# Optimization experiments

Hardware: AMD Instinct MI355X
Metric: run time of the kernel (lower is better)

## Reference

```python
import jax, jax.numpy as jnp
import numpy as np

D = 768
HEAD_SIZE = 64  # D / num_heads = 768 / 12

def setup_inputs() -> dict:
    key = jax.random.key(0)
    k1, k2, k3, k4 = jax.random.split(key, 4)
    ix = jax.random.normal(k1, (8, 4096, D), dtype=jnp.float32)
    # Linear(D, head_size, bias=False) weights; stored as [D, head_size] for x @ W
    scale = 1.0 / np.sqrt(D)
    Wk = jax.random.uniform(k2, (D, HEAD_SIZE), dtype=jnp.float32, minval=-scale, maxval=scale)
    Wq = jax.random.uniform(k3, (D, HEAD_SIZE), dtype=jnp.float32, minval=-scale, maxval=scale)
    Wv = jax.random.uniform(k4, (D, HEAD_SIZE), dtype=jnp.float32, minval=-scale, maxval=scale)
    return {"ix": ix, "Wk": Wk, "Wq": Wq, "Wv": Wv}

def reference(ix, Wk, Wq, Wv):
    # ix: [B, S, D]
    k = ix @ Wk  # [B, S, H]
    q = ix @ Wq  # [B, S, H]
    v = ix @ Wv  # [B, S, H]
    scale = 1.0 / jnp.sqrt(jnp.asarray(HEAD_SIZE, ix.dtype))
    wei = jnp.einsum('bsh,bth->bst', q, k) * scale  # [B, S, S]
    wei = jax.nn.softmax(wei, axis=-1)
    out = jnp.einsum('bst,bth->bsh', wei, v)  # [B, S, H]
    return out
```

## Files before the change

kernel.cpp:

```cpp
#include <hip/hip_runtime.h>
#include <hip/hip_bf16.h>

#define D_DIM 768
#define HS 64
#define SEQ 4096
#define NBATCH 8

typedef short bf8 __attribute__((ext_vector_type(8)));
typedef short bf4 __attribute__((ext_vector_type(4)));
typedef float f4 __attribute__((ext_vector_type(4)));

static __device__ __forceinline__ short f2b(float x) {
    __hip_bfloat16 h = __float2bfloat16(x);
    return __builtin_bit_cast(short, h);
}
static __device__ __forceinline__ unsigned pk2(float x, float y) {
    unsigned ux = __builtin_bit_cast(unsigned, x) + 0x8000u;
    unsigned uy = __builtin_bit_cast(unsigned, y) + 0x8000u;
    return __builtin_amdgcn_perm(uy, ux, 0x07060302u);
}

#if defined(__has_builtin)
#if __has_builtin(__builtin_amdgcn_exp2f)
#define EXP2F(x) __builtin_amdgcn_exp2f(x)
#endif
#endif
#ifndef EXP2F
#define EXP2F(x) exp2f(x)
#endif

__global__ __launch_bounds__(256) void wconv_kernel(
    const float* __restrict__ Wk, const float* __restrict__ Wq,
    const float* __restrict__ Wv, short* __restrict__ wt)
{
    int tid = blockIdx.x * 256 + threadIdx.x;
    int mat = tid / (D_DIM * HS);
    int rem = tid - mat * (D_DIM * HS);
    int k = rem >> 6;
    int n = rem & 63;
    const float* W = (mat == 0) ? Wk : (mat == 1) ? Wq : Wv;
    float scale = (mat == 1) ? 0.18033688011112042f : 1.0f;
    wt[(mat * HS + n) * D_DIM + k] = f2b(W[rem] * scale);
}

__global__ __launch_bounds__(256) void proj_kernel(
    const float* __restrict__ ix, const short* __restrict__ wt,
    short* __restrict__ qg, short* __restrict__ kg, short* __restrict__ vg)
{
    __shared__ short ixl[2][32 * 40];
    __shared__ short wtl[2][192 * 40];

    const int t = threadIdx.x;
    const int wave = t >> 6, lane = t & 63;
    const int m = lane & 15, quad = lane >> 4;
    const int m0 = blockIdx.x * 32;

    const int srow = t >> 3;
    const int skoff = (t & 7) * 4;

    f4 xr;
    bf8 wr0, wr1, wr2, wr3;

    auto load_chunk = [&](int c) {
        const float* px = ix + (m0 + srow) * D_DIM + c * 32 + skoff;
        xr = *(const f4*)px;
        if (t < 192) {
            const short* pw = wt + t * D_DIM + c * 32;
            wr0 = *(const bf8*)(pw);
            wr1 = *(const bf8*)(pw + 8);
            wr2 = *(const bf8*)(pw + 16);
            wr3 = *(const bf8*)(pw + 24);
        }
    };
    auto write_chunk = [&](int p) {
        bf4 xw;
        #pragma unroll
        for (int i = 0; i < 4; ++i) xw[i] = f2b(xr[i]);
        *(bf4*)(&ixl[p][srow * 40 + skoff]) = xw;
        if (t < 192) {
            *(bf8*)(&wtl[p][t * 40 + 0])  = wr0;
            *(bf8*)(&wtl[p][t * 40 + 8])  = wr1;
            *(bf8*)(&wtl[p][t * 40 + 16]) = wr2;
            *(bf8*)(&wtl[p][t * 40 + 24]) = wr3;
        }
    };

    f4 acc[2][3] = {};

    load_chunk(0); write_chunk(0); __syncthreads();

    for (int c = 0; c < 24; ++c) {
        const int p = c & 1;
        if (c + 1 < 24) load_chunk(c + 1);

        bf8 a0 = *(const bf8*)(&ixl[p][(m) * 40 + quad * 8]);
        bf8 a1 = *(const bf8*)(&ixl[p][(16 + m) * 40 + quad * 8]);
        bf8 bb[3];
        #pragma unroll
        for (int nt = 0; nt < 3; ++nt)
            bb[nt] = *(const bf8*)(&wtl[p][(wave * 48 + nt * 16 + m) * 40 + quad * 8]);
        #pragma unroll
        for (int nt = 0; nt < 3; ++nt) {
            acc[0][nt] = __builtin_amdgcn_mfma_f32_16x16x32_bf16(a0, bb[nt], acc[0][nt], 0, 0, 0);
            acc[1][nt] = __builtin_amdgcn_mfma_f32_16x16x32_bf16(a1, bb[nt], acc[1][nt], 0, 0, 0);
        }

        if (c + 1 < 24) { write_chunk((c + 1) & 1); __syncthreads(); }
    }

    #pragma unroll
    for (int mt = 0; mt < 2; ++mt) {
        const int row = m0 + mt * 16 + quad * 4;
        #pragma unroll
        for (int nt = 0; nt < 3; ++nt) {
            const int cb = wave * 48 + nt * 16;
            short* op = (cb < 64) ? kg : (cb < 128) ? qg : vg;
            const int n = (cb & 63) + m;
            #pragma unroll
            for (int r = 0; r < 4; ++r)
                op[(row + r) * HS + n] = f2b(acc[mt][nt][r]);
        }
    }
}

__global__ __launch_bounds__(256, 4) void attn_kernel(
    const short* __restrict__ qg, const short* __restrict__ kg,
    const short* __restrict__ vg, float* __restrict__ num0,
    float* __restrict__ num1, float* __restrict__ num2,
    float* __restrict__ num3, float* __restrict__ den0,
    float* __restrict__ den1, float* __restrict__ den2,
    float* __restrict__ den3)
{
    __shared__ short kl[2][64 * 72];
    __shared__ short vl[2][64 * 64];

    const int t = threadIdx.x;
    const int wave = t >> 6, lane = t & 63;
    const int m = lane & 15, quad = lane >> 4;

    const int flat = blockIdx.x;
    const int lg = (flat & 7) * 128 + (flat >> 3);
    const int qx = lg & 31;
    const int ks = (lg >> 5) & 3;
    const int b  = lg >> 7;

    const int rbase = b * SEQ;
    const int kbase = rbase + ks * (SEQ / 4);
    const int qw = qx * 128 + wave * 32;

    float* __restrict__ nump = (ks == 0) ? num0 : (ks == 1) ? num1 : (ks == 2) ? num2 : num3;
    float* __restrict__ denp = (ks == 0) ? den0 : (ks == 1) ? den1 : (ks == 2) ? den2 : den3;

    bf8 qf[2][2];
    #pragma unroll
    for (int nq = 0; nq < 2; ++nq)
        #pragma unroll
        for (int st = 0; st < 2; ++st)
            qf[nq][st] = *(const bf8*)(qg + (rbase + qw + nq * 16 + m) * HS + st * 32 + quad * 8);

    const int srow = t >> 2, soff = (t & 3) * 16;
    const int jp = t >> 3, dg = t & 7;
    const int j0 = jp * 2;
    const int jj = j0 & 31;
    const int gj = j0 >> 5;
    const int vq = (jj >> 2) & 3;
    const int vh = (jj >> 4) & 1;
    const int vb = (jj & 3) >> 1;
    const int vcol_base = vh * 4 + 2 * vb;
    const int vchunk_l = 4 * gj + vq;

    uint4 kr0, kr1, vr0, vr1;
    auto load_chunk = [&](int c) {
        const short* pk = kg + (kbase + c * 64 + srow) * HS + soff;
        kr0 = *(const uint4*)pk; kr1 = *(const uint4*)(pk + 8);
        const short* pv = vg + (kbase + c * 64 + j0) * HS + dg * 8;
        vr0 = *(const uint4*)pv; vr1 = *(const uint4*)(pv + HS);
    };
    auto write_chunk = [&](int p) {
        *(bf8*)(&kl[p][srow * 72 + soff])     = __builtin_bit_cast(bf8, kr0);
        *(bf8*)(&kl[p][srow * 72 + soff + 8]) = __builtin_bit_cast(bf8, kr1);
        bf8 v0 = __builtin_bit_cast(bf8, vr0), v1 = __builtin_bit_cast(bf8, vr1);
        #pragma unroll
        for (int i = 0; i < 8; ++i) {
            const int d = dg * 8 + i;
            const int chunk = vchunk_l ^ (i ^ dg);
            unsigned val = (unsigned short)v0[i] | ((unsigned)(unsigned short)v1[i] << 16);
            *(unsigned*)(&vl[p][d * 64 + chunk * 8 + vcol_base]) = val;
        }
    };

    f4 o[2][4] = {};
    float den[2] = {0.f, 0.f};

    load_chunk(0); write_chunk(0); __syncthreads();

    const int NCH = SEQ / 4 / 64;
    for (int c = 0; c < NCH; ++c) {
        const int p = c & 1;
        if (c + 1 < NCH) load_chunk(c + 1);

        #pragma unroll
        for (int g = 0; g < 2; ++g) {
            bf8 kA0 = *(const bf8*)(&kl[p][(g * 32 + m) * 72 + quad * 8]);
            bf8 kA1 = *(const bf8*)(&kl[p][(g * 32 + m) * 72 + 32 + quad * 8]);
            bf8 kB0 = *(const bf8*)(&kl[p][(g * 32 + 16 + m) * 72 + quad * 8]);
            bf8 kB1 = *(const bf8*)(&kl[p][(g * 32 + 16 + m) * 72 + 32 + quad * 8]);

            bf8 vf[4];
            #pragma unroll
            for (int dt = 0; dt < 4; ++dt) {
                const int row = dt * 16 + m;
                const int key = (m & 7) ^ (2 * dt + (m >> 3));
                const int chunk = (g * 4 + quad) ^ key;
                vf[dt] = *(const bf8*)(&vl[p][row * 64 + chunk * 8]);
            }

            #pragma unroll
            for (int nq = 0; nq < 2; ++nq) {
                f4 sa = {0.f, 0.f, 0.f, 0.f}, sb = {0.f, 0.f, 0.f, 0.f};
                sa = __builtin_amdgcn_mfma_f32_16x16x32_bf16(kA0, qf[nq][0], sa, 0, 0, 0);
                sa = __builtin_amdgcn_mfma_f32_16x16x32_bf16(kA1, qf[nq][1], sa, 0, 0, 0);
                sb = __builtin_amdgcn_mfma_f32_16x16x32_bf16(kB0, qf[nq][0], sb, 0, 0, 0);
                sb = __builtin_amdgcn_mfma_f32_16x16x32_bf16(kB1, qf[nq][1], sb, 0, 0, 0);
                float e0 = EXP2F(sa[0]), e1 = EXP2F(sa[1]), e2 = EXP2F(sa[2]), e3 = EXP2F(sa[3]);
                float e4 = EXP2F(sb[0]), e5 = EXP2F(sb[1]), e6 = EXP2F(sb[2]), e7 = EXP2F(sb[3]);
                den[nq] += ((e0 + e1) + (e2 + e3)) + ((e4 + e5) + (e6 + e7));
                uint4 pu;
                pu.x = pk2(e0, e1); pu.y = pk2(e2, e3);
                pu.z = pk2(e4, e5); pu.w = pk2(e6, e7);
                bf8 pf = __builtin_bit_cast(bf8, pu);
                #pragma unroll
                for (int dt = 0; dt < 4; ++dt)
                    o[nq][dt] = __builtin_amdgcn_mfma_f32_16x16x32_bf16(vf[dt], pf, o[nq][dt], 0, 0, 0);
            }
        }

        if (c + 1 < NCH) { write_chunk((c + 1) & 1); __syncthreads(); }
    }

    #pragma unroll
    for (int nq = 0; nq < 2; ++nq) {
        float d = den[nq];
        d += __shfl_xor(d, 16, 64);
        d += __shfl_xor(d, 32, 64);
        const int orow = rbase + qw + nq * 16 + m;
        if (quad == 0) denp[orow] = d;
        #pragma unroll
        for (int dt = 0; dt < 4; ++dt)
            *(f4*)(nump + orow * HS + dt * 16 + quad * 4) = o[nq][dt];
    }
}

__global__ __launch_bounds__(256) void reduce_kernel(
    float* __restrict__ out, const float* __restrict__ num1,
    const float* __restrict__ num2, const float* __restrict__ num3,
    const float* __restrict__ den0, const float* __restrict__ den1,
    const float* __restrict__ den2, const float* __restrict__ den3)
{
    const int gid = blockIdx.x * 256 + threadIdx.x;
    const int base = gid * 4;
    const int r = base >> 6;
    f4 n0 = *(const f4*)(out + base);
    f4 n1 = *(const f4*)(num1 + base);
    f4 n2 = *(const f4*)(num2 + base);
    f4 n3 = *(const f4*)(num3 + base);
    const float rs = 1.0f / ((den0[r] + den1[r]) + (den2[r] + den3[r]));
    f4 res;
    #pragma unroll
    for (int i = 0; i < 4; ++i) res[i] = ((n0[i] + n1[i]) + (n2[i] + n3[i])) * rs;
    *(f4*)(out + base) = res;
}

extern "C" void kernel_launch(void* const* d_in, const int* in_sizes, int n_in,
                              void* d_out, int out_size, void* d_ws, size_t ws_size,
                              hipStream_t stream) {
    const float* ix = (const float*)d_in[0];
    const float* Wk = (const float*)d_in[1];
    const float* Wq = (const float*)d_in[2];
    const float* Wv = (const float*)d_in[3];
    float* out = (float*)d_out;

    const size_t NQKV = (size_t)NBATCH * SEQ * HS;
    short* qg = (short*)d_ws;
    short* kg = qg + NQKV;
    short* vg = kg + NQKV;
    short* wt = vg + NQKV;
    char*  fbase = (char*)(wt + 3 * D_DIM * HS);
    float* num1 = (float*)fbase;
    float* num2 = num1 + NQKV;
    float* num3 = num2 + NQKV;
    float* den0 = num3 + NQKV;
    float* den1 = den0 + (size_t)NBATCH * SEQ;
    float* den2 = den1 + (size_t)NBATCH * SEQ;
    float* den3 = den2 + (size_t)NBATCH * SEQ;

    wconv_kernel<<<(3 * D_DIM * HS) / 256, 256, 0, stream>>>(Wk, Wq, Wv, wt);
    proj_kernel<<<(NBATCH * SEQ) / 32, 256, 0, stream>>>(ix, wt, qg, kg, vg);
    attn_kernel<<<1024, 256, 0, stream>>>(qg, kg, vg, out, num1, num2, num3,
                                          den0, den1, den2, den3);
    reduce_kernel<<<(int)(NQKV / (256 * 4)), 256, 0, stream>>>(
        out, num1, num2, num3, den0, den1, den2, den3);
}
```

Before: 249.4 us.

## Pre-tile projection weights for direct MFMA loads and double the K chunk

Result: faster. 219.7 us (-11.9%).

```diff
diff --git a/kernel.cpp b/kernel.cpp
--- a/kernel.cpp
+++ b/kernel.cpp
@@ -31,7 +31,7 @@
 
 __global__ __launch_bounds__(256) void wconv_kernel(
     const float* __restrict__ Wk, const float* __restrict__ Wq,
-    const float* __restrict__ Wv, short* __restrict__ wt)
+    const float* __restrict__ Wv, short* __restrict__ wt3)
 {
     int tid = blockIdx.x * 256 + threadIdx.x;
     int mat = tid / (D_DIM * HS);
@@ -40,15 +40,16 @@
     int n = rem & 63;
     const float* W = (mat == 0) ? Wk : (mat == 1) ? Wq : Wv;
     float scale = (mat == 1) ? 0.18033688011112042f : 1.0f;
-    wt[(mat * HS + n) * D_DIM + k] = f2b(W[rem] * scale);
+    int cc = mat * HS + n;
+    int c = k >> 5, q = (k >> 3) & 3, e = k & 7;
+    wt3[(c * 192 + cc) * 32 + q * 8 + e] = f2b(W[rem] * scale);
 }
 
 __global__ __launch_bounds__(256) void proj_kernel(
-    const float* __restrict__ ix, const short* __restrict__ wt,
+    const float* __restrict__ ix, const short* __restrict__ wt3,
     short* __restrict__ qg, short* __restrict__ kg, short* __restrict__ vg)
 {
-    __shared__ short ixl[2][32 * 40];
-    __shared__ short wtl[2][192 * 40];
+    __shared__ short ixl[2][32 * 72];
 
     const int t = threadIdx.x;
     const int wave = t >> 6, lane = t & 63;
@@ -56,56 +57,51 @@
     const int m0 = blockIdx.x * 32;
 
     const int srow = t >> 3;
-    const int skoff = (t & 7) * 4;
-
-    f4 xr;
-    bf8 wr0, wr1, wr2, wr3;
-
-    auto load_chunk = [&](int c) {
-        const float* px = ix + (m0 + srow) * D_DIM + c * 32 + skoff;
-        xr = *(const f4*)px;
-        if (t < 192) {
-            const short* pw = wt + t * D_DIM + c * 32;
-            wr0 = *(const bf8*)(pw);
-            wr1 = *(const bf8*)(pw + 8);
-            wr2 = *(const bf8*)(pw + 16);
-            wr3 = *(const bf8*)(pw + 24);
-        }
-    };
-    auto write_chunk = [&](int p) {
-        bf4 xw;
-        #pragma unroll
-        for (int i = 0; i < 4; ++i) xw[i] = f2b(xr[i]);
-        *(bf4*)(&ixl[p][srow * 40 + skoff]) = xw;
-        if (t < 192) {
-            *(bf8*)(&wtl[p][t * 40 + 0])  = wr0;
-            *(bf8*)(&wtl[p][t * 40 + 8])  = wr1;
-            *(bf8*)(&wtl[p][t * 40 + 16]) = wr2;
-            *(bf8*)(&wtl[p][t * 40 + 24]) = wr3;
-        }
-    };
-
+    const int skoff = (t & 7) * 8;
+
+    f4 xr0, xr1;
+    auto load_ix = [&](int c) {
+        const float* px = ix + (m0 + srow) * D_DIM + c * 64 + skoff;
+        xr0 = *(const f4*)px;
+        xr1 = *(const f4*)(px + 4);
+    };
+    auto write_ix = [&](int p) {
+        bf8 xw;
+        #pragma unroll
+        for (int i = 0; i < 4; ++i) { xw[i] = f2b(xr0[i]); xw[i + 4] = f2b(xr1[i]); }
+        *(bf8*)(&ixl[p][srow * 72 + skoff]) = xw;
+    };
+
+    const int colb = wave * 48;
     f4 acc[2][3] = {};
 
-    load_chunk(0); write_chunk(0); __syncthreads();
-
-    for (int c = 0; c < 24; ++c) {
+    load_ix(0); write_ix(0); __syncthreads();
+
+    for (int c = 0; c < 12; ++c) {
         const int p = c & 1;
-        if (c + 1 < 24) load_chunk(c + 1);
-
-        bf8 a0 = *(const bf8*)(&ixl[p][(m) * 40 + quad * 8]);
-        bf8 a1 = *(const bf8*)(&ixl[p][(16 + m) * 40 + quad * 8]);
-        bf8 bb[3];
-        #pragma unroll
-        for (int nt = 0; nt < 3; ++nt)
-            bb[nt] = *(const bf8*)(&wtl[p][(wave * 48 + nt * 16 + m) * 40 + quad * 8]);
+        if (c + 1 < 12) load_ix(c + 1);
+
+        bf8 b0[3], b1[3];
         #pragma unroll
         for (int nt = 0; nt < 3; ++nt) {
-            acc[0][nt] = __builtin_amdgcn_mfma_f32_16x16x32_bf16(a0, bb[nt], acc[0][nt], 0, 0, 0);
-            acc[1][nt] = __builtin_amdgcn_mfma_f32_16x16x32_bf16(a1, bb[nt], acc[1][nt], 0, 0, 0);
-        }
-
-        if (c + 1 < 24) { write_chunk((c + 1) & 1); __syncthreads(); }
+            const short* pw = wt3 + ((2 * c) * 192 + colb + nt * 16 + m) * 32 + quad * 8;
+            b0[nt] = *(const bf8*)pw;
+            b1[nt] = *(const bf8*)(pw + 192 * 32);
+        }
+        bf8 a0 = *(const bf8*)(&ixl[p][m * 72 + quad * 8]);
+        bf8 a1 = *(const bf8*)(&ixl[p][m * 72 + 32 + quad * 8]);
+        bf8 a2 = *(const bf8*)(&ixl[p][(16 + m) * 72 + quad * 8]);
+        bf8 a3 = *(const bf8*)(&ixl[p][(16 + m) * 72 + 32 + quad * 8]);
+
+        #pragma unroll
+        for (int nt = 0; nt < 3; ++nt) {
+            acc[0][nt] = __builtin_amdgcn_mfma_f32_16x16x32_bf16(a0, b0[nt], acc[0][nt], 0, 0, 0);
+            acc[0][nt] = __builtin_amdgcn_mfma_f32_16x16x32_bf16(a1, b1[nt], acc[0][nt], 0, 0, 0);
+            acc[1][nt] = __builtin_amdgcn_mfma_f32_16x16x32_bf16(a2, b0[nt], acc[1][nt], 0, 0, 0);
+            acc[1][nt] = __builtin_amdgcn_mfma_f32_16x16x32_bf16(a3, b1[nt], acc[1][nt], 0, 0, 0);
+        }
+
+        if (c + 1 < 12) { write_ix((c + 1) & 1); __syncthreads(); }
     }
 
     #pragma unroll
@@ -113,7 +109,7 @@
         const int row = m0 + mt * 16 + quad * 4;
         #pragma unroll
         for (int nt = 0; nt < 3; ++nt) {
-            const int cb = wave * 48 + nt * 16;
+            const int cb = colb + nt * 16;
             short* op = (cb < 64) ? kg : (cb < 128) ? qg : vg;
             const int n = (cb & 63) + m;
             #pragma unroll
@@ -284,8 +280,8 @@
     short* qg = (short*)d_ws;
     short* kg = qg + NQKV;
     short* vg = kg + NQKV;
-    short* wt = vg + NQKV;
-    char*  fbase = (char*)(wt + 3 * D_DIM * HS);
+    short* wt3 = vg + NQKV;
+    char*  fbase = (char*)(wt3 + 24 * 192 * 32);
     float* num1 = (float*)fbase;
     float* num2 = num1 + NQKV;
     float* num3 = num2 + NQKV;
@@ -294,8 +290,8 @@
     float* den2 = den1 + (size_t)NBATCH * SEQ;
     float* den3 = den2 + (size_t)NBATCH * SEQ;
 
-    wconv_kernel<<<(3 * D_DIM * HS) / 256, 256, 0, stream>>>(Wk, Wq, Wv, wt);
-    proj_kernel<<<(NBATCH * SEQ) / 32, 256, 0, stream>>>(ix, wt, qg, kg, vg);
+    wconv_kernel<<<(3 * D_DIM * HS) / 256, 256, 0, stream>>>(Wk, Wq, Wv, wt3);
+    proj_kernel<<<(NBATCH * SEQ) / 32, 256, 0, stream>>>(ix, wt3, qg, kg, vg);
     attn_kernel<<<1024, 256, 0, stream>>>(qg, kg, vg, out, num1, num2, num3,
                                           den0, den1, den2, den3);
     reduce_kernel<<<(int)(NQKV / (256 * 4)), 256, 0, stream>>>(
```
